# Performance work log

Measured on AMD Instinct MI355X. Metric: run time of the kernel, lower is better.

## Reference

```python
import jax, jax.numpy as jnp
import numpy as np

N_EMBD = 2048
N_HEAD = 16
HEAD_DIM = N_EMBD // N_HEAD
LORA_R = 8
LORA_ALPHA = 1.0
LORA_SCALING = LORA_ALPHA / LORA_R


def setup_inputs() -> dict:
    key = jax.random.key(0)
    ks = jax.random.split(key, 10)
    B, T = 4, 2048
    init = LORA_ALPHA / LORA_R
    return {
        "x": jax.random.normal(ks[0], (B, T, N_EMBD), dtype=jnp.float32),
        "W_attn": jax.random.normal(ks[1], (N_EMBD, 3 * N_EMBD), dtype=jnp.float32) * 0.02,
        "b_attn": jnp.zeros((3 * N_EMBD,), dtype=jnp.float32),
        "lora_A_q": jax.random.normal(ks[2], (N_EMBD, LORA_R), dtype=jnp.float32) * init,
        "lora_B_q": jax.random.normal(ks[3], (LORA_R, N_EMBD), dtype=jnp.float32) * init,
        "lora_A_k": jax.random.normal(ks[4], (N_EMBD, LORA_R), dtype=jnp.float32) * init,
        "lora_B_k": jax.random.normal(ks[5], (LORA_R, N_EMBD), dtype=jnp.float32) * init,
        "W_proj": jax.random.normal(ks[6], (N_EMBD, N_EMBD), dtype=jnp.float32) * 0.02,
        "b_proj": jnp.zeros((N_EMBD,), dtype=jnp.float32),
    }


def _rotate_half(x):
    # torch: x1 = x[..., ::2]; x2 = x[..., 1::2]; cat((-x2, x1), -1)
    x1 = x[..., ::2]
    x2 = x[..., 1::2]
    return jnp.concatenate([-x2, x1], axis=-1)


def _rope_cos_sin(T, dtype):
    inv_freq = 1.0 / (10000.0 ** (jnp.arange(0, HEAD_DIM, 2, dtype=jnp.float32) / HEAD_DIM))
    t = jnp.arange(T, dtype=jnp.float32)
    freqs = jnp.einsum("i,j->ij", t, inv_freq)            # [T, D/2]
    emb = jnp.concatenate([freqs, freqs], axis=-1)          # [T, D]
    return jnp.cos(emb).astype(dtype), jnp.sin(emb).astype(dtype)


def reference(x, W_attn, b_attn, lora_A_q, lora_B_q, lora_A_k, lora_B_k, W_proj, b_proj):
    B, T, C = x.shape
    qkv = x @ W_attn + b_attn                                # [B,T,3C]
    q, k, v = jnp.split(qkv, 3, axis=2)
    # LoRA additions on q, k (applied to attn outputs, per module)
    q = q + (q @ lora_A_q) @ lora_B_q * LORA_SCALING
    k = k + (k @ lora_A_k) @ lora_B_k * LORA_SCALING

    def to_heads(z):
        return z.reshape(B, T, N_HEAD, HEAD_DIM).transpose(0, 2, 1, 3)  # [B,H,T,D]

    q, k, v = to_heads(q), to_heads(k), to_heads(v)
    cos, sin = _rope_cos_sin(T, x.dtype)                     # [T,D] each
    q = q * cos + _rotate_half(q) * sin
    k = k * cos + _rotate_half(k) * sin

    scale = 1.0 / jnp.sqrt(jnp.asarray(HEAD_DIM, dtype=x.dtype))
    scores = jnp.einsum("bhqd,bhkd->bhqk", q, k) * scale     # [B,H,T,T]
    causal = jnp.tril(jnp.ones((T, T), dtype=bool))
    scores = jnp.where(causal, scores, jnp.finfo(x.dtype).min)
    attn = jax.nn.softmax(scores, axis=-1)
    y = jnp.einsum("bhqk,bhkd->bhqd", attn, v)               # [B,H,T,D]
    y = y.transpose(0, 2, 1, 3).reshape(B, T, C)
    return y @ W_proj + b_proj
```

## Files before the change

kernel.cpp:

```cpp
#include <hip/hip_runtime.h>
#include <stdint.h>


typedef __attribute__((ext_vector_type(8))) short short8;
typedef __attribute__((ext_vector_type(4))) short short4v;
typedef __attribute__((ext_vector_type(4))) float floatx4;

__device__ __forceinline__ float bf2f(short h) {
  union { unsigned int u; float f; } v;
  v.u = ((unsigned int)(unsigned short)h) << 16;
  return v.f;
}
__device__ __forceinline__ short f2bf(float f) {
  unsigned int u = __float_as_uint(f);
  unsigned int r = (u + 0x7FFFu + ((u >> 16) & 1u)) >> 16;
  return (short)r;
}

__device__ __forceinline__ void gload_lds16(const short* g, short* l) {
  __builtin_amdgcn_global_load_lds(
      (const __attribute__((address_space(1))) unsigned int*)g,
      (__attribute__((address_space(3))) unsigned int*)l, 16, 0, 0);
}

__device__ __forceinline__ void store_out(float* p, float v) { *p = v; }
__device__ __forceinline__ void store_out(short* p, float v) { *p = f2bf(v); }

__device__ __forceinline__ int xcd_swz(int orig, int nwg) {
  int q = nwg >> 3;
  return (orig & 7) * q + (orig >> 3);
}

__global__ void k_f2b(const float* __restrict__ in, short* __restrict__ out, int n8) {
  int i = blockIdx.x * 256 + threadIdx.x;
  if (i >= n8) return;
  const float4* p = (const float4*)in + (size_t)i * 2;
  float4 a = p[0], b = p[1];
  short8 v;
  v[0] = f2bf(a.x); v[1] = f2bf(a.y); v[2] = f2bf(a.z); v[3] = f2bf(a.w);
  v[4] = f2bf(b.x); v[5] = f2bf(b.y); v[6] = f2bf(b.z); v[7] = f2bf(b.w);
  *(short8*)(out + (size_t)i * 8) = v;
}

__global__ void k_wT(const float* __restrict__ W, short* __restrict__ WT, int K, int N) {
  __shared__ float tile[32][33];
  int n0 = blockIdx.x * 32, k0 = blockIdx.y * 32;
  int tx = threadIdx.x, ty = threadIdx.y;
  #pragma unroll
  for (int i = 0; i < 4; i++)
    tile[ty + i * 8][tx] = W[(size_t)(k0 + ty + i * 8) * N + n0 + tx];
  __syncthreads();
  #pragma unroll
  for (int i = 0; i < 4; i++)
    WT[(size_t)(n0 + ty + i * 8) * K + k0 + tx] = f2bf(tile[tx][ty + i * 8]);
}

__global__ void k_ropetab(float* __restrict__ ct, float* __restrict__ st) {
  int t = blockIdx.x, j = threadIdx.x;
  float invf = powf(10000.0f, -(float)(2 * j) / 128.0f);
  float ang = (float)t * invf;
  ct[t * 64 + j] = cosf(ang);
  st[t * 64 + j] = sinf(ang);
}


#define GBAR __builtin_amdgcn_s_barrier();

#define GPH(QR, QC, BUF) { \
    const short* Ab_ = lds + (BUF) * 32768; \
    const short* Bb_ = Ab_ + 16384; \
    short8 afr[4][2]; short8 bfr[2][2]; \
    _Pragma("unroll") for (int m_ = 0; m_ < 4; m_++) \
    _Pragma("unroll") for (int kk_ = 0; kk_ < 2; kk_++) { \
      int sA_ = ((QR) * 2 + wm) * 8192 + (m_ * 16 + c16) * 128 + kk_ * 64 + g * 16; \
      afr[m_][kk_] = *(const short8*)(Ab_ + ((sA_ ^ swzk) >> 1)); \
    } \
    _Pragma("unroll") for (int n_ = 0; n_ < 2; n_++) \
    _Pragma("unroll") for (int kk_ = 0; kk_ < 2; kk_++) { \
      int sB_ = ((QC) * 4 + wn) * 4096 + (n_ * 16 + c16) * 128 + kk_ * 64 + g * 16; \
      bfr[n_][kk_] = *(const short8*)(Bb_ + ((sB_ ^ swzk) >> 1)); \
    }

#define GMM(QR, QC) \
    __builtin_amdgcn_s_barrier(); \
    __builtin_amdgcn_s_setprio(1); \
    _Pragma("unroll") for (int kk_ = 0; kk_ < 2; kk_++) \
    _Pragma("unroll") for (int m_ = 0; m_ < 4; m_++) \
    _Pragma("unroll") for (int n_ = 0; n_ < 2; n_++) \
      acc[(QR) * 4 + m_][(QC) * 2 + n_] = __builtin_amdgcn_mfma_f32_16x16x32_bf16( \
          afr[m_][kk_], bfr[n_][kk_], acc[(QR) * 4 + m_][(QC) * 2 + n_], 0, 0, 0); \
    __builtin_amdgcn_s_setprio(0); \
  }

template <typename OutT>
__global__ __launch_bounds__(512, 2) void k_gemm8(
    const short* __restrict__ A, const short* __restrict__ BT,
    const float* __restrict__ bias, OutT* __restrict__ C,
    int M, int N, int K)
{
  __shared__ __attribute__((aligned(16))) short lds[65536];
  const int tid = threadIdx.x;
  const int w = tid >> 6, l = tid & 63;
  const int g = l >> 4, c16 = l & 15;
  const int wm = w >> 2, wn = w & 3;
  const int swzk = (c16 & 7) << 4;

  const int nwg = gridDim.x * gridDim.y;
  const int wg = xcd_swz(blockIdx.y * gridDim.x + blockIdx.x, nwg);
  const int bm = wg % gridDim.x, bn = wg / gridDim.x;

  const short* Ablk = A + (size_t)bm * 256 * K;
  const short* Bblk = BT + (size_t)bn * 256 * K;

  floatx4 acc[8][4];
  #pragma unroll
  for (int i = 0; i < 8; i++)
    #pragma unroll
    for (int j = 0; j < 4; j++)
      acc[i][j] = (floatx4){0.f, 0.f, 0.f, 0.f};

  const int NT = K >> 6;
  const int L = NT >> 1;

  auto stageA = [&](int b, int h, int t) {
    short* dst = lds + b * 32768;
    int k0 = t * 64;
    #pragma unroll
    for (int j = 0; j < 2; j++) {
      int P = h * 2 + j;
      int sL = P * 8192 + tid * 16;
      int q = sL ^ (((sL >> 7) & 7) << 4);
      int row = (((((P & 1) << 1) | (P >> 1))) << 6) + ((sL >> 7) & 63);
      gload_lds16(Ablk + (size_t)row * K + k0 + ((q & 127) >> 1), dst + (sL >> 1));
    }
  };
  auto stageB = [&](int b, int h, int t) {
    short* dst = lds + b * 32768 + 16384;
    int k0 = t * 64;
    #pragma unroll
    for (int j = 0; j < 2; j++) {
      int sL = (h * 4 + 2 * j) * 4096 + tid * 16;
      int pos = sL >> 12;
      int q = sL ^ (((sL >> 7) & 7) << 4);
      int row = (((pos & 3) * 2 + (pos >> 2)) << 5) + ((sL >> 7) & 31);
      gload_lds16(Bblk + (size_t)row * K + k0 + ((q & 127) >> 1), dst + (sL >> 1));
    }
  };

  stageA(0, 0, 0); stageB(0, 0, 0); stageA(0, 1, 0); stageB(0, 1, 0);
  stageA(1, 0, 1); stageB(1, 0, 1); stageA(1, 1, 1); stageB(1, 1, 1);
  asm volatile("s_waitcnt vmcnt(8)" ::: "memory");
  __builtin_amdgcn_s_barrier();

  #pragma unroll 1
  for (int i = 0; i < L; i++) {
    const int t2 = 2 * i + 2, t3 = 2 * i + 3;

    GPH(0, 0, 0) if (i > 0) stageA(1, 1, 2 * i + 1); GMM(0, 0) GBAR
    GPH(0, 1, 0) if (i > 0) stageB(1, 1, 2 * i + 1); GMM(0, 1) GBAR
    GPH(1, 0, 0) if (t2 < NT) stageA(0, 0, t2);      GMM(1, 0) GBAR
    GPH(1, 1, 0) if (t2 < NT) stageB(0, 0, t2);      GMM(1, 1)
    if (t2 < NT) { asm volatile("s_waitcnt vmcnt(4)" ::: "memory"); }
    else         { asm volatile("s_waitcnt vmcnt(0)" ::: "memory"); }
    GBAR
    GPH(0, 0, 1) if (t2 < NT) stageA(0, 1, t2);      GMM(0, 0) GBAR
    GPH(0, 1, 1) if (t2 < NT) stageB(0, 1, t2);      GMM(0, 1) GBAR
    GPH(1, 0, 1) if (t3 < NT) stageA(1, 0, t3);      GMM(1, 0) GBAR
    GPH(1, 1, 1) if (t3 < NT) stageB(1, 0, t3);      GMM(1, 1)
    if (t3 < NT) { asm volatile("s_waitcnt vmcnt(4)" ::: "memory"); }
    else         { asm volatile("s_waitcnt vmcnt(0)" ::: "memory"); }
    GBAR
  }

  #pragma unroll
  for (int qr = 0; qr < 2; qr++)
    #pragma unroll
    for (int qc = 0; qc < 2; qc++)
      #pragma unroll
      for (int m = 0; m < 4; m++)
        #pragma unroll
        for (int n = 0; n < 2; n++) {
          int col = bn * 256 + wn * 64 + qc * 32 + n * 16 + c16;
          float bv = bias[col];
          #pragma unroll
          for (int r = 0; r < 4; r++) {
            size_t row = (size_t)bm * 256 + wm * 128 + qr * 64 + m * 16 + g * 4 + r;
            store_out(C + row * (size_t)N + col, acc[qr * 4 + m][qc * 2 + n][r] + bv);
          }
        }
}

__global__ __launch_bounds__(256, 2) void k_lorarope(
    short* __restrict__ qkv, const float* __restrict__ Aq, const float* __restrict__ Ak,
    const float* __restrict__ Bq, const float* __restrict__ Bk,
    const float* __restrict__ ct, const float* __restrict__ st)
{
  __shared__ float Bs[8 * 2048];
  __shared__ short Ls[2048];
  __shared__ float red[4][8];
  const int u = threadIdx.x;
  const int which = blockIdx.y;
  const float* Am = which ? Ak : Aq;
  const float* Bm = which ? Bk : Bq;
  const float qs = which ? 1.0f : 0.08838834764831845f;

  #pragma unroll
  for (int i = 0; i < 16; i++) {
    int idx = (i * 256 + u) * 4;
    *(float4*)(Bs + idx) = *(const float4*)(Bm + idx);
  }
  float Areg[8][8];
  #pragma unroll
  for (int e = 0; e < 8; e++) {
    float4 a0 = *(const float4*)(Am + (size_t)(u * 8 + e) * 8);
    float4 a1 = *(const float4*)(Am + (size_t)(u * 8 + e) * 8 + 4);
    Areg[e][0] = a0.x; Areg[e][1] = a0.y; Areg[e][2] = a0.z; Areg[e][3] = a0.w;
    Areg[e][4] = a1.x; Areg[e][5] = a1.y; Areg[e][6] = a1.z; Areg[e][7] = a1.w;
  }
  __syncthreads();

  const int wv = u >> 6, l = u & 63;
  const int h = u >> 4, j0 = (u & 15) * 4;
  const int base = h * 128;
  const int t0 = blockIdx.x * 32;

  for (int tt = 0; tt < 32; tt++) {
    const int tok = t0 + tt;
    const int trow = tok & 2047;
    short* row = qkv + (size_t)tok * 6144 + which * 2048;

    __syncthreads();

    short8 q8 = *(const short8*)(row + u * 8);
    *(short8*)(Ls + u * 8) = q8;
    float part[8];
    #pragma unroll
    for (int r = 0; r < 8; r++) part[r] = 0.f;
    #pragma unroll
    for (int e = 0; e < 8; e++) {
      float qv = bf2f(q8[e]);
      #pragma unroll
      for (int r = 0; r < 8; r++) part[r] += qv * Areg[e][r];
    }
    #pragma unroll
    for (int r = 0; r < 8; r++)
      for (int off = 32; off > 0; off >>= 1)
        part[r] += __shfl_xor(part[r], off);
    if (l == 0) {
      #pragma unroll
      for (int r = 0; r < 8; r++) red[wv][r] = part[r];
    }
    __syncthreads();

    float Tr[8];
    #pragma unroll
    for (int r = 0; r < 8; r++)
      Tr[r] = (red[0][r] + red[1][r] + red[2][r] + red[3][r]) * 0.125f;

    float4 cv = *(const float4*)(ct + trow * 64 + j0);
    float4 sv = *(const float4*)(st + trow * 64 + j0);
    short4v qa4 = *(const short4v*)(Ls + base + j0);
    short4v qb4 = *(const short4v*)(Ls + base + 64 + j0);
    short8 qeo = *(const short8*)(Ls + base + 2 * j0);

    float o1[4], o2[4];
    #pragma unroll
    for (int j = 0; j < 4; j++) {
      float da = 0.f, db = 0.f, de = 0.f, dd = 0.f;
      #pragma unroll
      for (int r = 0; r < 8; r++) {
        const float* Br = Bs + r * 2048 + base;
        da += Tr[r] * Br[j0 + j];
        db += Tr[r] * Br[64 + j0 + j];
        de += Tr[r] * Br[2 * (j0 + j)];
        dd += Tr[r] * Br[2 * (j0 + j) + 1];
      }
      float qa = bf2f(qa4[j]) + da;
      float qb = bf2f(qb4[j]) + db;
      float qe = bf2f(qeo[2 * j]) + de;
      float qo = bf2f(qeo[2 * j + 1]) + dd;
      float c = ((const float*)&cv)[j], s = ((const float*)&sv)[j];
      o1[j] = (qa * c - qo * s) * qs;
      o2[j] = (qb * c + qe * s) * qs;
    }
    short4v w1, w2;
    #pragma unroll
    for (int j = 0; j < 4; j++) { w1[j] = f2bf(o1[j]); w2[j] = f2bf(o2[j]); }
    *(short4v*)(row + base + j0) = w1;
    *(short4v*)(row + base + 64 + j0) = w2;
  }
}

__global__ void k_vt(const short* __restrict__ qkv, short* __restrict__ vT) {
  __shared__ short tile[32][33];
  int bh = blockIdx.z, b = bh >> 4, h = bh & 15;
  int t0 = blockIdx.x * 32, d0 = blockIdx.y * 32;
  int tx = threadIdx.x, ty = threadIdx.y;
  #pragma unroll
  for (int i = 0; i < 4; i++) {
    int tt = t0 + ty + i * 8;
    tile[ty + i * 8][tx] = qkv[(size_t)(b * 2048 + tt) * 6144 + 4096 + h * 128 + d0 + tx];
  }
  __syncthreads();
  #pragma unroll
  for (int i = 0; i < 4; i++) {
    int d = d0 + ty + i * 8;
    vT[((size_t)bh * 128 + d) * 2048 + t0 + tx] = tile[tx][ty + i * 8];
  }
}

__global__ __launch_bounds__(256, 2) void k_attn(
    const short* __restrict__ qkv, const short* __restrict__ vT, short* __restrict__ y)
{
  __shared__ __attribute__((aligned(16))) short Ks[64 * 136];
  __shared__ __attribute__((aligned(16))) short Vs[128 * 72];
  __shared__ __attribute__((aligned(16))) short Ps[4 * 32 * 72];
  const int bh = blockIdx.y, b = bh >> 4, h = bh & 15;
  const int t = threadIdx.x, w = t >> 6, l = t & 63, g = l >> 4, c16 = l & 15;

  const int skr = t >> 2, sc0 = (t & 3) * 32;
  const int svd = t >> 1, sv0 = (t & 1) * 32;
  const short* kbase = qkv + (size_t)(b * 2048) * 6144 + 2048 + h * 128;
  const short* vbase = vT + (size_t)bh * 128 * 2048;
  short* Pw = Ps + w * (32 * 72);

  for (int pass = 0; pass < 2; pass++) {
    const int qt = pass ? (15 - (int)blockIdx.x) : (int)blockIdx.x;

    short8 qf[2][4];
    #pragma unroll
    for (int m = 0; m < 2; m++) {
      size_t goff = (size_t)(b * 2048 + qt * 128 + w * 32 + m * 16 + c16) * 6144 + h * 128;
      #pragma unroll
      for (int kf = 0; kf < 4; kf++)
        qf[m][kf] = *(const short8*)(qkv + goff + kf * 32 + 8 * g);
    }

    floatx4 o[2][8];
    float mrow[2][4], lrow[2][4];
    #pragma unroll
    for (int m = 0; m < 2; m++) {
      #pragma unroll
      for (int nf = 0; nf < 8; nf++) o[m][nf] = (floatx4){0.f, 0.f, 0.f, 0.f};
      #pragma unroll
      for (int r = 0; r < 4; r++) { mrow[m][r] = -1e30f; lrow[m][r] = 0.f; }
    }

    const int ntiles = 2 * qt + 2;

    short8 kreg[4], vreg[4];
    #pragma unroll
    for (int ii = 0; ii < 4; ii++) {
      kreg[ii] = *(const short8*)(kbase + (size_t)skr * 6144 + sc0 + ii * 8);
      vreg[ii] = *(const short8*)(vbase + (size_t)svd * 2048 + sv0 + ii * 8);
    }

    for (int kt = 0; kt < ntiles; kt++) {
      __syncthreads();
      #pragma unroll
      for (int ii = 0; ii < 4; ii++) {
        *(short8*)(Ks + skr * 136 + sc0 + ii * 8) = kreg[ii];
        *(short8*)(Vs + svd * 72 + sv0 + ii * 8) = vreg[ii];
      }
      __syncthreads();

      if (kt + 1 < ntiles) {
        #pragma unroll
        for (int ii = 0; ii < 4; ii++) {
          kreg[ii] = *(const short8*)(kbase + (size_t)((kt + 1) * 64 + skr) * 6144 + sc0 + ii * 8);
          vreg[ii] = *(const short8*)(vbase + (size_t)svd * 2048 + (kt + 1) * 64 + sv0 + ii * 8);
        }
      }

      floatx4 sc[2][4];
      #pragma unroll
      for (int m = 0; m < 2; m++)
        #pragma unroll
        for (int nf = 0; nf < 4; nf++) sc[m][nf] = (floatx4){0.f, 0.f, 0.f, 0.f};
      __builtin_amdgcn_s_setprio(1);
      #pragma unroll
      for (int kf = 0; kf < 4; kf++)
        #pragma unroll
        for (int nf = 0; nf < 4; nf++) {
          short8 kb = *(const short8*)(Ks + (nf * 16 + c16) * 136 + kf * 32 + 8 * g);
          sc[0][nf] = __builtin_amdgcn_mfma_f32_16x16x32_bf16(qf[0][kf], kb, sc[0][nf], 0, 0, 0);
          sc[1][nf] = __builtin_amdgcn_mfma_f32_16x16x32_bf16(qf[1][kf], kb, sc[1][nf], 0, 0, 0);
        }
      __builtin_amdgcn_s_setprio(0);

      if (kt >= 2 * qt) {
        #pragma unroll
        for (int m = 0; m < 2; m++)
          #pragma unroll
          for (int nf = 0; nf < 4; nf++) {
            int key = kt * 64 + nf * 16 + c16;
            #pragma unroll
            for (int r = 0; r < 4; r++) {
              int qr = qt * 128 + w * 32 + m * 16 + g * 4 + r;
              if (key > qr) sc[m][nf][r] = -1e30f;
            }
          }
      }

      float rmv[2][4];
      float need = -1e30f;
      #pragma unroll
      for (int m = 0; m < 2; m++)
        #pragma unroll
        for (int r = 0; r < 4; r++) {
          float rm = fmaxf(fmaxf(sc[m][0][r], sc[m][1][r]), fmaxf(sc[m][2][r], sc[m][3][r]));
          rm = fmaxf(rm, __shfl_xor(rm, 1));
          rm = fmaxf(rm, __shfl_xor(rm, 2));
          rm = fmaxf(rm, __shfl_xor(rm, 4));
          rm = fmaxf(rm, __shfl_xor(rm, 8));
          rmv[m][r] = rm;
          need = fmaxf(need, rm - mrow[m][r]);
        }
      if (!__all(need <= 8.0f)) {
        #pragma unroll
        for (int m = 0; m < 2; m++)
          #pragma unroll
          for (int r = 0; r < 4; r++) {
            float mn = fmaxf(mrow[m][r], rmv[m][r]);
            float al = __expf(mrow[m][r] - mn);
            mrow[m][r] = mn;
            lrow[m][r] *= al;
            #pragma unroll
            for (int nf = 0; nf < 8; nf++) o[m][nf] *= al;
          }
      }
      #pragma unroll
      for (int m = 0; m < 2; m++)
        #pragma unroll
        for (int r = 0; r < 4; r++) {
          float rs = 0.f;
          float pr[4];
          #pragma unroll
          for (int nf = 0; nf < 4; nf++) {
            float p = __expf(sc[m][nf][r] - mrow[m][r]);
            pr[nf] = p;
            rs += p;
          }
          rs += __shfl_xor(rs, 1);
          rs += __shfl_xor(rs, 2);
          rs += __shfl_xor(rs, 4);
          rs += __shfl_xor(rs, 8);
          lrow[m][r] += rs;
          #pragma unroll
          for (int nf = 0; nf < 4; nf++)
            Pw[(m * 16 + g * 4 + r) * 72 + nf * 16 + c16] = f2bf(pr[nf]);
        }

      asm volatile("s_waitcnt lgkmcnt(0)" ::: "memory");
      __builtin_amdgcn_sched_barrier(0);

      short8 pa[2][2];
      #pragma unroll
      for (int m = 0; m < 2; m++)
        #pragma unroll
        for (int kf = 0; kf < 2; kf++)
          pa[m][kf] = *(const short8*)(Pw + (m * 16 + c16) * 72 + kf * 32 + 8 * g);
      __builtin_amdgcn_s_setprio(1);
      #pragma unroll
      for (int kf = 0; kf < 2; kf++)
        #pragma unroll
        for (int nf = 0; nf < 8; nf++) {
          short8 vb = *(const short8*)(Vs + (nf * 16 + c16) * 72 + kf * 32 + 8 * g);
          o[0][nf] = __builtin_amdgcn_mfma_f32_16x16x32_bf16(pa[0][kf], vb, o[0][nf], 0, 0, 0);
          o[1][nf] = __builtin_amdgcn_mfma_f32_16x16x32_bf16(pa[1][kf], vb, o[1][nf], 0, 0, 0);
        }
      __builtin_amdgcn_s_setprio(0);
    }

    #pragma unroll
    for (int m = 0; m < 2; m++) {
      float ri[4];
      #pragma unroll
      for (int r = 0; r < 4; r++) ri[r] = 1.0f / lrow[m][r];
      size_t yr0 = (size_t)(b * 2048 + qt * 128 + w * 32 + m * 16 + g * 4);
      #pragma unroll
      for (int nf = 0; nf < 8; nf++) {
        int col = h * 128 + nf * 16 + c16;
        #pragma unroll
        for (int r = 0; r < 4; r++)
          y[(yr0 + r) * 2048 + col] = f2bf(o[m][nf][r] * ri[r]);
      }
    }
  }
}

extern "C" void kernel_launch(void* const* d_in, const int* in_sizes, int n_in,
                              void* d_out, int out_size, void* d_ws, size_t ws_size,
                              hipStream_t stream) {
  (void)in_sizes; (void)n_in; (void)out_size; (void)ws_size;
  const float* x      = (const float*)d_in[0];
  const float* W_attn = (const float*)d_in[1];
  const float* b_attn = (const float*)d_in[2];
  const float* Aq     = (const float*)d_in[3];
  const float* Bq     = (const float*)d_in[4];
  const float* Ak     = (const float*)d_in[5];
  const float* Bk     = (const float*)d_in[6];
  const float* W_proj = (const float*)d_in[7];
  const float* b_proj = (const float*)d_in[8];

  char* ws = (char*)d_ws;
  short* xb  = (short*)(ws + 0);
  short* WTa = (short*)(ws + 33554432);
  short* WTp = (short*)(ws + 58720256);
  short* qkv = (short*)(ws + 67108864);
  float* ct  = (float*)(ws + 168296448);
  float* st  = (float*)(ws + 168820736);
  short* vT  = (short*)(ws + 169345024);
  short* y   = xb;

  k_f2b<<<8192, 256, 0, stream>>>(x, xb, 2097152);
  k_wT<<<dim3(192, 64), dim3(32, 8), 0, stream>>>(W_attn, WTa, 2048, 6144);
  k_wT<<<dim3(64, 64), dim3(32, 8), 0, stream>>>(W_proj, WTp, 2048, 2048);
  k_ropetab<<<2048, 64, 0, stream>>>(ct, st);
  k_gemm8<short><<<dim3(32, 24), 512, 0, stream>>>(xb, WTa, b_attn, qkv, 8192, 6144, 2048);
  k_lorarope<<<dim3(256, 2), 256, 0, stream>>>(qkv, Aq, Ak, Bq, Bk, ct, st);
  k_vt<<<dim3(64, 4, 64), dim3(32, 8), 0, stream>>>(qkv, vT);
  k_attn<<<dim3(8, 64), 256, 0, stream>>>(qkv, vT, y);
  k_gemm8<float><<<dim3(32, 8), 512, 0, stream>>>(y, WTp, b_proj, (float*)d_out, 8192, 2048, 2048);
}
```

Before: 579.6 us.

## Reuse A/B register fragments across GEMM quadrants and reschedule LDS staging

The GEMM main loop used to reload both A and B fragments from LDS for each of its four sub-tile quadrants. It now keeps A fragments in registers across the two column quadrants and holds two sets of B fragments for reuse across the row quadrants, which roughly halves LDS reads per k-step. The global-to-LDS prefetch order and the vmcnt wait thresholds are reshuffled to match the new read order. In exchange it uses more VGPRs for the extra B fragments, and the revised staging order must keep buffer reuse race-free.

```diff
diff --git a/kernel.cpp b/kernel.cpp
--- a/kernel.cpp
+++ b/kernel.cpp
@@ -66,31 +66,29 @@
 
 #define GBAR __builtin_amdgcn_s_barrier();
 
-#define GPH(QR, QC, BUF) { \
-    const short* Ab_ = lds + (BUF) * 32768; \
-    const short* Bb_ = Ab_ + 16384; \
-    short8 afr[4][2]; short8 bfr[2][2]; \
+#define RDA(QR) \
     _Pragma("unroll") for (int m_ = 0; m_ < 4; m_++) \
     _Pragma("unroll") for (int kk_ = 0; kk_ < 2; kk_++) { \
       int sA_ = ((QR) * 2 + wm) * 8192 + (m_ * 16 + c16) * 128 + kk_ * 64 + g * 16; \
-      afr[m_][kk_] = *(const short8*)(Ab_ + ((sA_ ^ swzk) >> 1)); \
-    } \
+      afr[m_][kk_] = *(const short8*)(Ab + ((sA_ ^ swzk) >> 1)); \
+    }
+
+#define RDB(QC, DST) \
     _Pragma("unroll") for (int n_ = 0; n_ < 2; n_++) \
     _Pragma("unroll") for (int kk_ = 0; kk_ < 2; kk_++) { \
       int sB_ = ((QC) * 4 + wn) * 4096 + (n_ * 16 + c16) * 128 + kk_ * 64 + g * 16; \
-      bfr[n_][kk_] = *(const short8*)(Bb_ + ((sB_ ^ swzk) >> 1)); \
-    }
-
-#define GMM(QR, QC) \
+      DST[n_][kk_] = *(const short8*)(Bb + ((sB_ ^ swzk) >> 1)); \
+    }
+
+#define MM(QR, QC, BF) \
     __builtin_amdgcn_s_barrier(); \
     __builtin_amdgcn_s_setprio(1); \
     _Pragma("unroll") for (int kk_ = 0; kk_ < 2; kk_++) \
     _Pragma("unroll") for (int m_ = 0; m_ < 4; m_++) \
     _Pragma("unroll") for (int n_ = 0; n_ < 2; n_++) \
       acc[(QR) * 4 + m_][(QC) * 2 + n_] = __builtin_amdgcn_mfma_f32_16x16x32_bf16( \
-          afr[m_][kk_], bfr[n_][kk_], acc[(QR) * 4 + m_][(QC) * 2 + n_], 0, 0, 0); \
-    __builtin_amdgcn_s_setprio(0); \
-  }
+          afr[m_][kk_], BF[n_][kk_], acc[(QR) * 4 + m_][(QC) * 2 + n_], 0, 0, 0); \
+    __builtin_amdgcn_s_setprio(0);
 
 template <typename OutT>
 __global__ __launch_bounds__(512, 2) void k_gemm8(
@@ -155,21 +153,38 @@
   #pragma unroll 1
   for (int i = 0; i < L; i++) {
     const int t2 = 2 * i + 2, t3 = 2 * i + 3;
-
-    GPH(0, 0, 0) if (i > 0) stageA(1, 1, 2 * i + 1); GMM(0, 0) GBAR
-    GPH(0, 1, 0) if (i > 0) stageB(1, 1, 2 * i + 1); GMM(0, 1) GBAR
-    GPH(1, 0, 0) if (t2 < NT) stageA(0, 0, t2);      GMM(1, 0) GBAR
-    GPH(1, 1, 0) if (t2 < NT) stageB(0, 0, t2);      GMM(1, 1)
-    if (t2 < NT) { asm volatile("s_waitcnt vmcnt(4)" ::: "memory"); }
-    else         { asm volatile("s_waitcnt vmcnt(0)" ::: "memory"); }
-    GBAR
-    GPH(0, 0, 1) if (t2 < NT) stageA(0, 1, t2);      GMM(0, 0) GBAR
-    GPH(0, 1, 1) if (t2 < NT) stageB(0, 1, t2);      GMM(0, 1) GBAR
-    GPH(1, 0, 1) if (t3 < NT) stageA(1, 0, t3);      GMM(1, 0) GBAR
-    GPH(1, 1, 1) if (t3 < NT) stageB(1, 0, t3);      GMM(1, 1)
-    if (t3 < NT) { asm volatile("s_waitcnt vmcnt(4)" ::: "memory"); }
-    else         { asm volatile("s_waitcnt vmcnt(0)" ::: "memory"); }
-    GBAR
+    short8 afr[4][2], bfr0[2][2], bfr1[2][2];
+
+    {
+      const short* Ab = lds;
+      const short* Bb = lds + 16384;
+      RDA(0) RDB(0, bfr0) if (i > 0) stageA(1, 1, 2 * i + 1);
+      MM(0, 0, bfr0) GBAR
+      RDB(1, bfr1) if (t2 < NT) stageA(0, 0, t2);
+      MM(0, 1, bfr1) GBAR
+      RDA(1) if (t2 < NT) stageB(0, 0, t2);
+      MM(1, 0, bfr0) GBAR
+      if (t2 < NT) stageB(0, 1, t2);
+      MM(1, 1, bfr1)
+      if (t2 < NT) { asm volatile("s_waitcnt vmcnt(6)" ::: "memory"); }
+      else         { asm volatile("s_waitcnt vmcnt(0)" ::: "memory"); }
+      GBAR
+    }
+    {
+      const short* Ab = lds + 32768;
+      const short* Bb = lds + 49152;
+      RDA(0) RDB(0, bfr0) if (t2 < NT) stageA(0, 1, t2);
+      MM(0, 0, bfr0) GBAR
+      RDB(1, bfr1) if (t3 < NT) stageA(1, 0, t3);
+      MM(0, 1, bfr1) GBAR
+      RDA(1) if (t3 < NT) stageB(1, 0, t3);
+      MM(1, 0, bfr0) GBAR
+      if (t3 < NT) stageB(1, 1, t3);
+      MM(1, 1, bfr1)
+      if (t3 < NT) { asm volatile("s_waitcnt vmcnt(6)" ::: "memory"); }
+      else         { asm volatile("s_waitcnt vmcnt(0)" ::: "memory"); }
+      GBAR
+    }
   }
 
   #pragma unroll
```

After: 549.9 us. -5.1%, faster.
